# Kernel tuning notes

Measured on AMD Instinct MI355X. Metric: run time of the kernel, lower is better.

The kernel has to match this reference:

```python
import jax, jax.numpy as jnp
import numpy as np

EMB = 1024   # emb_dim
HID = 1024   # hid_dim (must equal EMB for the original router to be well-formed)
E = 16       # num_experts
K = 2        # num_active_experts


def setup_inputs() -> dict:
    key = jax.random.key(0)
    ks = jax.random.split(key, 5)
    s_in = (2.0 / EMB) ** 0.5
    s_hid = (2.0 / HID) ** 0.5
    x = jax.random.normal(ks[0], (2, 4096, EMB), dtype=jnp.float32)
    w_gate = jax.random.normal(ks[1], (EMB, E), dtype=jnp.float32) * s_in
    w1 = jax.random.normal(ks[2], (E, EMB, HID), dtype=jnp.float32) * s_in  # exp_1 weights
    w2 = jax.random.normal(ks[3], (E, EMB, HID), dtype=jnp.float32) * s_in  # exp_2 weights
    wc = jax.random.normal(ks[4], (E, HID, EMB), dtype=jnp.float32) * s_hid  # contr weights
    return {"x": x, "w_gate": w_gate, "w1": w1, "w2": w2, "wc": wc}


def reference(x, w_gate, w1, w2, wc):
    b, s, d = x.shape
    xf = x.reshape(-1, d)                      # [N, d]
    n = xf.shape[0]
    # Router: softmax over expert logits, then top-k (no renormalization of topk scores,
    # matching the torch module).
    probs = jax.nn.softmax(xf @ w_gate, axis=-1)   # [N, E]
    scores, idx = jax.lax.top_k(probs, K)          # [N, K]
    # Dense gate matrix: gate[t, e] = score if e in topk(t) else 0 (topk indices distinct).
    gates = jnp.zeros((n, E), dtype=xf.dtype).at[jnp.arange(n)[:, None], idx].set(scores)
    # Loop (scan) over the fixed expert count; each expert runs a SwiGLU MLP over all
    # tokens and its output is combined with the (mostly zero) gate weights. This is the
    # standard dense-combine MoE reference: same math as the masked torch loop since
    # unselected tokens get gate 0.
    def body(acc, ws):
        w1e, w2e, wce, ge = ws                 # [d,h], [d,h], [h,d], [N]
        h = jax.nn.silu(xf @ w1e) * (xf @ w2e)  # [N, h]
        return acc + ge[:, None] * (h @ wce), None

    out, _ = jax.lax.scan(body, jnp.zeros_like(xf), (w1, w2, wc, gates.T))
    return out.reshape(b, s, d)
```

## Files before the change

### kernel.cpp

```cpp
#include <hip/hip_runtime.h>
#include <hip/hip_bf16.h>
#include <stdint.h>

#define EMB 1024
#define HID 1024
#define NE 16
#define NTOK 8192
#define NSLOT (NTOK * 2)
#define BM 128
#define BN 128
#define BK 32

typedef __bf16 bf16;
typedef __bf16 bf16x8 __attribute__((ext_vector_type(8)));
typedef __bf16 bf16x4 __attribute__((ext_vector_type(4)));
typedef float f32x4 __attribute__((ext_vector_type(4)));

#define GLOAD16(g, l)                                                        \
  __builtin_amdgcn_global_load_lds(                                          \
      (const __attribute__((address_space(1))) void*)(g),                    \
      (__attribute__((address_space(3))) void*)(l), 16, 0, 0)

__global__ void transpose_cvt3(const float* __restrict__ w1, const float* __restrict__ w2,
                               const float* __restrict__ wcs, bf16* __restrict__ w1t,
                               bf16* __restrict__ w2t, bf16* __restrict__ wct) {
  __shared__ float tile[32][33];
  int zz = blockIdx.z;
  const float* s; bf16* d;
  if (zz < 16)      { s = w1;  d = w1t; }
  else if (zz < 32) { s = w2;  d = w2t; }
  else              { s = wcs; d = wct; }
  int z = zz & 15;
  int x0 = blockIdx.x << 5, y0 = blockIdx.y << 5;
  s += (size_t)z * EMB * HID;
  d += (size_t)z * EMB * HID;
  int tx = threadIdx.x, ty = threadIdx.y;
#pragma unroll
  for (int i = 0; i < 32; i += 8)
    tile[ty + i][tx] = s[(size_t)(y0 + ty + i) * 1024 + x0 + tx];
  __syncthreads();
#pragma unroll
  for (int i = 0; i < 32; i += 8)
    d[(size_t)(x0 + ty + i) * 1024 + y0 + tx] = (bf16)tile[tx][ty + i];
}

__global__ void wgT_k(const float* __restrict__ wg, float* __restrict__ wgT) {
  int f = blockIdx.x * 256 + threadIdx.x;
  int d = f >> 4, e = f & 15;
  wgT[e * 1024 + d] = wg[f];
}

__launch_bounds__(1024)
__global__ void router_k(const float* __restrict__ x, const float* __restrict__ wgT,
                         bf16* __restrict__ xb,
                         int* __restrict__ tokexp, float* __restrict__ tokgate) {
  __shared__ float wgs[NE * 1024];
  for (int i = threadIdx.x; i < 4096; i += 1024)
    ((float4*)wgs)[i] = ((const float4*)wgT)[i];
  __syncthreads();

  int t = blockIdx.x * 16 + (threadIdx.x >> 6);
  int lane = threadIdx.x & 63;
  const float* xr = x + (size_t)t * EMB;

  float acc[NE];
#pragma unroll
  for (int e = 0; e < NE; e++) acc[e] = 0.f;

#pragma unroll
  for (int c = 0; c < 4; c++) {
    float4 xv = ((const float4*)xr)[c * 64 + lane];
    int dbase = c * 256 + lane * 4;
    bf16x4 o;
    o[0] = (bf16)xv.x; o[1] = (bf16)xv.y; o[2] = (bf16)xv.z; o[3] = (bf16)xv.w;
    *(bf16x4*)(xb + (size_t)t * EMB + dbase) = o;
#pragma unroll
    for (int e = 0; e < NE; e++) {
      float4 wv = *(const float4*)&wgs[e * 1024 + dbase];
      acc[e] += xv.x * wv.x + xv.y * wv.y + xv.z * wv.z + xv.w * wv.w;
    }
  }
#pragma unroll
  for (int e = 0; e < NE; e++) {
#pragma unroll
    for (int s = 32; s > 0; s >>= 1) acc[e] += __shfl_xor(acc[e], s);
  }
  if (lane == 0) {
    float m = acc[0];
#pragma unroll
    for (int e = 1; e < NE; e++) m = fmaxf(m, acc[e]);
    float p[NE]; float sum = 0.f;
#pragma unroll
    for (int e = 0; e < NE; e++) { p[e] = __expf(acc[e] - m); sum += p[e]; }
    float inv = 1.f / sum;
#pragma unroll
    for (int e = 0; e < NE; e++) p[e] *= inv;
    int i1 = 0;
#pragma unroll
    for (int e = 1; e < NE; e++) if (p[e] > p[i1]) i1 = e;
    int i2 = (i1 == 0) ? 1 : 0;
#pragma unroll
    for (int e = 0; e < NE; e++) if (e != i1 && p[e] > p[i2]) i2 = e;
    tokexp[2 * t] = i1; tokexp[2 * t + 1] = i2;
    tokgate[2 * t] = p[i1]; tokgate[2 * t + 1] = p[i2];
  }
}

__global__ void hist_k(const int* __restrict__ tokexp, int* __restrict__ blockcnt) {
  __shared__ int h[NE];
  int tid = threadIdx.x;
  if (tid < NE) h[tid] = 0;
  __syncthreads();
  int e = tokexp[blockIdx.x * 256 + tid];
  atomicAdd(&h[e], 1);
  __syncthreads();
  if (tid < NE) blockcnt[blockIdx.x * NE + tid] = h[tid];
}

__global__ void scan_k(const int* __restrict__ blockcnt, int* __restrict__ cnt,
                       int* __restrict__ eoff, int* __restrict__ blockoff) {
  __shared__ int scnt[NE], soff[NE];
  int t = threadIdx.x;
  if (t < NE) {
    int s = 0;
    for (int b = 0; b < 64; b++) s += blockcnt[b * NE + t];
    scnt[t] = s;
    cnt[t] = s;
  }
  __syncthreads();
  if (t == 0) {
    int s = 0;
    for (int e = 0; e < NE; e++) { soff[e] = s; eoff[e] = s; s += scnt[e]; }
  }
  __syncthreads();
  if (t < NE) {
    int run = soff[t];
    for (int b = 0; b < 64; b++) { blockoff[b * NE + t] = run; run += blockcnt[b * NE + t]; }
  }
}

__global__ void assign_k(const int* __restrict__ tokexp, const float* __restrict__ tokgate,
                         const int* __restrict__ blockoff, int* __restrict__ rowtok,
                         float* __restrict__ rowgate) {
  __shared__ int wavecnt[4][NE];
  __shared__ int waveoff[4][NE];
  int tid = threadIdx.x;
  int w = tid >> 6, lane = tid & 63;
  int s = blockIdx.x * 256 + tid;
  int e = tokexp[s];
  int rank = 0;
  unsigned long long ltmask = (1ull << lane) - 1ull;
#pragma unroll
  for (int ee = 0; ee < NE; ee++) {
    unsigned long long bal = __ballot(e == ee);
    if (e == ee) rank = __popcll(bal & ltmask);
    if (lane == ee) wavecnt[w][ee] = __popcll(bal);
  }
  __syncthreads();
  if (tid < 64) {
    int ww = tid >> 4, ee = tid & 15;
    int off = 0;
    for (int p = 0; p < ww; p++) off += wavecnt[p][ee];
    waveoff[ww][ee] = off;
  }
  __syncthreads();
  int pos = blockoff[blockIdx.x * NE + e] + waveoff[w][e] + rank;
  rowtok[pos] = s >> 1;
  rowgate[pos] = tokgate[s];
}

__launch_bounds__(256, 2)
__global__ void gemm1_k(const bf16* __restrict__ xb, const bf16* __restrict__ w1t,
                        const bf16* __restrict__ w2t, const int* __restrict__ cnt,
                        const int* __restrict__ eoff, const int* __restrict__ rowtok,
                        bf16* __restrict__ H) {
  int id = blockIdx.x;
  int nid = (id & 7) * 1024 + (id >> 3);
  int e = nid >> 9;
  int rem = nid & 511;
  int m0 = (rem >> 3) * BM;
  int n0 = (rem & 7) * BN;
  int n_e = cnt[e];
  if (m0 >= n_e) return;
  int base = eoff[e];

  __shared__ __align__(16) bf16 sA[2][BM * BK];
  __shared__ __align__(16) bf16 sB1[2][BN * BK];
  __shared__ __align__(16) bf16 sB2[2][BN * BK];

  int tid = threadIdx.x;
  int lane = tid & 63;
  int w = tid >> 6;
  int wr = (w >> 1) << 6;
  int wc = (w & 1) << 6;

  int srow = tid >> 2;
  int kc = (tid & 3) << 3;

  const bf16 *ag0, *ag1;
  {
    int gi0 = base + m0 + srow;
    int gi1 = base + m0 + 64 + srow;
    gi0 = gi0 < NSLOT ? gi0 : NSLOT - 1;
    gi1 = gi1 < NSLOT ? gi1 : NSLOT - 1;
    ag0 = xb + (size_t)rowtok[gi0] * EMB + kc;
    ag1 = xb + (size_t)rowtok[gi1] * EMB + kc;
  }
  const bf16* b1g = w1t + ((size_t)e * HID + n0 + srow) * EMB + kc;
  const bf16* b2g = w2t + ((size_t)e * HID + n0 + srow) * EMB + kc;
  const size_t B64 = (size_t)64 * EMB;

  char* lA  = (char*)sA  + w * 1024;
  char* lB1 = (char*)sB1 + w * 1024;
  char* lB2 = (char*)sB2 + w * 1024;

#define G1STAGE(k0, b) do {                                                  \
    char* _A = lA + (b) * 8192; char* _B1 = lB1 + (b) * 8192;                \
    char* _B2 = lB2 + (b) * 8192;                                            \
    GLOAD16(ag0 + (k0), _A);                                                 \
    GLOAD16(ag1 + (k0), _A + 4096);                                          \
    GLOAD16(b1g + (k0), _B1);                                                \
    GLOAD16(b1g + B64 + (k0), _B1 + 4096);                                   \
    GLOAD16(b2g + (k0), _B2);                                                \
    GLOAD16(b2g + B64 + (k0), _B2 + 4096);                                   \
  } while (0)

  f32x4 acc1[4][4] = {};
  f32x4 acc2[4][4] = {};

  int ra = (wr + (lane & 15)) * BK + ((lane >> 4) << 3);
  int rb = (wc + (lane & 15)) * BK + ((lane >> 4) << 3);

  G1STAGE(0, 0);
  for (int t = 0; t < EMB / BK; t++) {
    int cur = t & 1;
    if (t < EMB / BK - 1) {
      G1STAGE((t + 1) * BK, cur ^ 1);
      asm volatile("s_waitcnt vmcnt(6)" ::: "memory");
    } else {
      asm volatile("s_waitcnt vmcnt(0)" ::: "memory");
    }
    __builtin_amdgcn_s_barrier();

    bf16x8 af[4], b1f[4], b2f[4];
#pragma unroll
    for (int m = 0; m < 4; m++) af[m] = *(const bf16x8*)&sA[cur][ra + m * 16 * BK];
#pragma unroll
    for (int n = 0; n < 4; n++) {
      b1f[n] = *(const bf16x8*)&sB1[cur][rb + n * 16 * BK];
      b2f[n] = *(const bf16x8*)&sB2[cur][rb + n * 16 * BK];
    }
#pragma unroll
    for (int m = 0; m < 4; m++)
#pragma unroll
      for (int n = 0; n < 4; n++) {
        acc1[m][n] = __builtin_amdgcn_mfma_f32_16x16x32_bf16(af[m], b1f[n], acc1[m][n], 0, 0, 0);
        acc2[m][n] = __builtin_amdgcn_mfma_f32_16x16x32_bf16(af[m], b2f[n], acc2[m][n], 0, 0, 0);
      }
    __builtin_amdgcn_s_barrier();
  }
#undef G1STAGE

  int rf = wr + ((lane >> 4) << 2);
  int cf = n0 + wc + (lane & 15);
#pragma unroll
  for (int m = 0; m < 4; m++) {
#pragma unroll
    for (int n = 0; n < 4; n++) {
#pragma unroll
      for (int b = 0; b < 4; b++) {
        int gr = m0 + rf + m * 16 + b;
        if (gr < n_e) {
          float c1 = acc1[m][n][b];
          float c2 = acc2[m][n][b];
          float h = c1 * c2 / (1.f + __expf(-c1));
          H[(size_t)(base + gr) * HID + cf + n * 16] = (bf16)h;
        }
      }
    }
  }
}

__launch_bounds__(256, 3)
__global__ void gemm2_k(const bf16* __restrict__ H, const bf16* __restrict__ wct,
                        const int* __restrict__ cnt, const int* __restrict__ eoff,
                        const int* __restrict__ rowtok, const float* __restrict__ rowgate,
                        float* __restrict__ out) {
  int id = blockIdx.x;
  int nid = (id & 7) * 1024 + (id >> 3);
  int e = nid >> 9;
  int rem = nid & 511;
  int m0 = (rem >> 3) * BM;
  int n0 = (rem & 7) * BN;
  int n_e = cnt[e];
  if (m0 >= n_e) return;
  int base = eoff[e];

  __shared__ __align__(16) bf16 sA[2][BM * BK];
  __shared__ __align__(16) bf16 sB[2][BN * BK];

  int tid = threadIdx.x;
  int lane = tid & 63;
  int w = tid >> 6;
  int wr = (w >> 1) << 6;
  int wc = (w & 1) << 6;

  int srow = tid >> 2;
  int kc = (tid & 3) << 3;

  const bf16 *ag0, *ag1;
  {
    int gi0 = base + m0 + srow;
    int gi1 = base + m0 + 64 + srow;
    gi0 = gi0 < NSLOT ? gi0 : NSLOT - 1;
    gi1 = gi1 < NSLOT ? gi1 : NSLOT - 1;
    ag0 = H + (size_t)gi0 * HID + kc;
    ag1 = H + (size_t)gi1 * HID + kc;
  }
  const bf16* bg = wct + ((size_t)e * EMB + n0 + srow) * HID + kc;
  const size_t B64 = (size_t)64 * HID;

  char* lA = (char*)sA + w * 1024;
  char* lB = (char*)sB + w * 1024;

#define G2STAGE(k0, b) do {                                                  \
    char* _A = lA + (b) * 8192; char* _B = lB + (b) * 8192;                  \
    GLOAD16(ag0 + (k0), _A);                                                 \
    GLOAD16(ag1 + (k0), _A + 4096);                                          \
    GLOAD16(bg + (k0), _B);                                                  \
    GLOAD16(bg + B64 + (k0), _B + 4096);                                     \
  } while (0)

  f32x4 acc[4][4] = {};

  int ra = (wr + (lane & 15)) * BK + ((lane >> 4) << 3);
  int rb = (wc + (lane & 15)) * BK + ((lane >> 4) << 3);

  G2STAGE(0, 0);
  for (int t = 0; t < HID / BK; t++) {
    int cur = t & 1;
    if (t < HID / BK - 1) {
      G2STAGE((t + 1) * BK, cur ^ 1);
      asm volatile("s_waitcnt vmcnt(4)" ::: "memory");
    } else {
      asm volatile("s_waitcnt vmcnt(0)" ::: "memory");
    }
    __builtin_amdgcn_s_barrier();

    bf16x8 af[4], bfr[4];
#pragma unroll
    for (int m = 0; m < 4; m++) af[m] = *(const bf16x8*)&sA[cur][ra + m * 16 * BK];
#pragma unroll
    for (int n = 0; n < 4; n++) bfr[n] = *(const bf16x8*)&sB[cur][rb + n * 16 * BK];
#pragma unroll
    for (int m = 0; m < 4; m++)
#pragma unroll
      for (int n = 0; n < 4; n++)
        acc[m][n] = __builtin_amdgcn_mfma_f32_16x16x32_bf16(af[m], bfr[n], acc[m][n], 0, 0, 0);
    __builtin_amdgcn_s_barrier();
  }
#undef G2STAGE

  int rf = wr + ((lane >> 4) << 2);
  int cf = n0 + wc + (lane & 15);
#pragma unroll
  for (int m = 0; m < 4; m++) {
#pragma unroll
    for (int b = 0; b < 4; b++) {
      int gr = m0 + rf + m * 16 + b;
      if (gr < n_e) {
        int idx = base + gr;
        int tok = rowtok[idx];
        float g = rowgate[idx];
        float* orow = out + (size_t)tok * EMB + cf;
#pragma unroll
        for (int n = 0; n < 4; n++)
          atomicAdd(orow + n * 16, g * acc[m][n][b]);
      }
    }
  }
}

extern "C" void kernel_launch(void* const* d_in, const int* in_sizes, int n_in,
                              void* d_out, int out_size, void* d_ws, size_t ws_size,
                              hipStream_t stream) {
  const float* x  = (const float*)d_in[0];
  const float* wg = (const float*)d_in[1];
  const float* w1 = (const float*)d_in[2];
  const float* w2 = (const float*)d_in[3];
  const float* wc = (const float*)d_in[4];
  float* out = (float*)d_out;

  const size_t WELEM = (size_t)NE * EMB * HID;
  bf16* w1t  = (bf16*)d_ws;
  bf16* w2t  = w1t + WELEM;
  bf16* wct  = w2t + WELEM;
  bf16* xb   = wct + WELEM;
  bf16* Hbuf = xb + (size_t)NTOK * EMB;
  int* cnt      = (int*)(Hbuf + (size_t)NSLOT * HID);
  int* eoff     = cnt + 16;
  int* blockcnt = eoff + 16;
  int* blockoff = blockcnt + 64 * 16;
  int* tokexp   = blockoff + 64 * 16;
  float* tokgate = (float*)(tokexp + NSLOT);
  int* rowtok    = (int*)(tokgate + NSLOT);
  float* rowgate = (float*)(rowtok + NSLOT);
  float* wgT     = rowgate + NSLOT;

  hipMemsetAsync(out, 0, (size_t)out_size * sizeof(float), stream);

  dim3 tb(32, 8), tg(32, 32, 48);
  transpose_cvt3<<<tg, tb, 0, stream>>>(w1, w2, wc, w1t, w2t, wct);
  wgT_k<<<64, 256, 0, stream>>>(wg, wgT);
  router_k<<<NTOK / 16, 1024, 0, stream>>>(x, wgT, xb, tokexp, tokgate);
  hist_k<<<NSLOT / 256, 256, 0, stream>>>(tokexp, blockcnt);
  scan_k<<<1, 64, 0, stream>>>(blockcnt, cnt, eoff, blockoff);
  assign_k<<<NSLOT / 256, 256, 0, stream>>>(tokexp, tokgate, blockoff, rowtok, rowgate);
  gemm1_k<<<8192, 256, 0, stream>>>(xb, w1t, w2t, cnt, eoff, rowtok, Hbuf);
  gemm2_k<<<8192, 256, 0, stream>>>(Hbuf, wct, cnt, eoff, rowtok, rowgate, out);
}
```

Baseline: 308.8 us.

## Swizzle GEMM LDS layout and vectorize weight transpose-convert kernel

Two changes. The weight transpose/convert kernel now uses 64x64 tiles with float4 loads, a bf16 LDS tile, and 16-byte bf16x8 stores, aiming to cut memory transactions in a pass that streams about 200MB of fp32 weights. Both expert GEMMs apply an XOR swizzle to the 16-byte chunk column used when writing A/B tiles into LDS and when reading MFMA fragments, to reduce LDS bank conflicts. The swizzle must match exactly between the global_load_lds write pattern and the fragment reads; a mismatch would corrupt the results.

```diff
diff --git a/kernel.cpp b/kernel.cpp
--- a/kernel.cpp
+++ b/kernel.cpp
@@ -24,24 +24,38 @@
 __global__ void transpose_cvt3(const float* __restrict__ w1, const float* __restrict__ w2,
                                const float* __restrict__ wcs, bf16* __restrict__ w1t,
                                bf16* __restrict__ w2t, bf16* __restrict__ wct) {
-  __shared__ float tile[32][33];
+  __shared__ bf16 tile[64][68];
   int zz = blockIdx.z;
   const float* s; bf16* d;
   if (zz < 16)      { s = w1;  d = w1t; }
   else if (zz < 32) { s = w2;  d = w2t; }
   else              { s = wcs; d = wct; }
   int z = zz & 15;
-  int x0 = blockIdx.x << 5, y0 = blockIdx.y << 5;
   s += (size_t)z * EMB * HID;
   d += (size_t)z * EMB * HID;
-  int tx = threadIdx.x, ty = threadIdx.y;
-#pragma unroll
-  for (int i = 0; i < 32; i += 8)
-    tile[ty + i][tx] = s[(size_t)(y0 + ty + i) * 1024 + x0 + tx];
-  __syncthreads();
-#pragma unroll
-  for (int i = 0; i < 32; i += 8)
-    d[(size_t)(x0 + ty + i) * 1024 + y0 + tx] = (bf16)tile[tx][ty + i];
+  int k0 = blockIdx.y << 6, n0 = blockIdx.x << 6;
+  int t = threadIdx.x;
+
+  int r = t >> 4, c4 = t & 15;
+#pragma unroll
+  for (int i = 0; i < 4; i++) {
+    int row = r + (i << 4);
+    float4 v = *(const float4*)&s[(size_t)(k0 + row) * 1024 + n0 + (c4 << 2)];
+    bf16x4 o;
+    o[0] = (bf16)v.x; o[1] = (bf16)v.y; o[2] = (bf16)v.z; o[3] = (bf16)v.w;
+    *(bf16x4*)&tile[row][c4 << 2] = o;
+  }
+  __syncthreads();
+
+  int r8 = t >> 3, ch = t & 7;
+#pragma unroll
+  for (int i = 0; i < 2; i++) {
+    int on = r8 + (i << 5);
+    bf16x8 v;
+#pragma unroll
+    for (int j = 0; j < 8; j++) v[j] = tile[(ch << 3) + j][on];
+    *(bf16x8*)&d[(size_t)(n0 + on) * 1024 + k0 + (ch << 3)] = v;
+  }
 }
 
 __global__ void wgT_k(const float* __restrict__ wg, float* __restrict__ wgT) {
@@ -168,6 +182,7 @@
   rowtok[pos] = s >> 1;
   rowgate[pos] = tokgate[s];
 }
+
 
 __launch_bounds__(256, 2)
 __global__ void gemm1_k(const bf16* __restrict__ xb, const bf16* __restrict__ w1t,
@@ -195,7 +210,7 @@
   int wc = (w & 1) << 6;
 
   int srow = tid >> 2;
-  int kc = (tid & 3) << 3;
+  int kc = (((tid & 3) ^ ((tid >> 3) & 3)) << 3);
 
   const bf16 *ag0, *ag1;
   {
@@ -228,8 +243,9 @@
   f32x4 acc1[4][4] = {};
   f32x4 acc2[4][4] = {};
 
-  int ra = (wr + (lane & 15)) * BK + ((lane >> 4) << 3);
-  int rb = (wc + (lane & 15)) * BK + ((lane >> 4) << 3);
+  int ch = ((lane >> 4) ^ ((lane >> 1) & 3)) << 3;
+  int ra = (wr + (lane & 15)) * BK + ch;
+  int rb = (wc + (lane & 15)) * BK + ch;
 
   G1STAGE(0, 0);
   for (int t = 0; t < EMB / BK; t++) {
@@ -306,7 +322,7 @@
   int wc = (w & 1) << 6;
 
   int srow = tid >> 2;
-  int kc = (tid & 3) << 3;
+  int kc = (((tid & 3) ^ ((tid >> 3) & 3)) << 3);
 
   const bf16 *ag0, *ag1;
   {
@@ -333,8 +349,9 @@
 
   f32x4 acc[4][4] = {};
 
-  int ra = (wr + (lane & 15)) * BK + ((lane >> 4) << 3);
-  int rb = (wc + (lane & 15)) * BK + ((lane >> 4) << 3);
+  int ch = ((lane >> 4) ^ ((lane >> 1) & 3)) << 3;
+  int ra = (wr + (lane & 15)) * BK + ch;
+  int rb = (wc + (lane & 15)) * BK + ch;
 
   G2STAGE(0, 0);
   for (int t = 0; t < HID / BK; t++) {
@@ -409,8 +426,8 @@
 
   hipMemsetAsync(out, 0, (size_t)out_size * sizeof(float), stream);
 
-  dim3 tb(32, 8), tg(32, 32, 48);
-  transpose_cvt3<<<tg, tb, 0, stream>>>(w1, w2, wc, w1t, w2t, wct);
+  dim3 tg(16, 16, 48);
+  transpose_cvt3<<<tg, 256, 0, stream>>>(w1, w2, wc, w1t, w2t, wct);
   wgT_k<<<64, 256, 0, stream>>>(wg, wgT);
   router_k<<<NTOK / 16, 1024, 0, stream>>>(x, wgT, xb, tokexp, tokgate);
   hist_k<<<NSLOT / 256, 256, 0, stream>>>(tokexp, blockcnt);
```

New measurement: 302.9 us. About the same (-1.9%).
